# Optimization experiments

Hardware: AMD Instinct MI355X
Metric: run time of the kernel (lower is better)

Reference implementation:

```python
import jax, jax.numpy as jnp
import numpy as np

B, C, RES, N_ANGLES = 32, 16, 128, 64


def setup_inputs() -> dict:
    key = jax.random.key(0)
    k1, k2, k3 = jax.random.split(key, 3)
    x = jax.random.normal(k1, (B, C, RES, RES), dtype=jnp.float32)
    # torch-radon setup: angles = np.linspace(0, 2*pi, 64)
    angles = jnp.linspace(0.0, 2.0 * np.pi, N_ANGLES).astype(jnp.float32)
    # Conv2d(16, 1, 1) params (kaiming-ish scale)
    conv_w = jax.random.normal(k2, (1, C, 1, 1), dtype=jnp.float32) * (1.0 / np.sqrt(C))
    conv_b = jax.random.normal(k3, (1,), dtype=jnp.float32) * 0.01
    return {"x": x, "angles": angles, "conv_w": conv_w, "conv_b": conv_b}


def _radon(x, angles):
    # x: (B, C, H, W) -> sinogram (B, C, n_angles, det_count)
    H = x.shape[-2]
    W = x.shape[-1]
    center = (H - 1) / 2.0
    # detector positions s and ray-integration positions t, in pixel units, centered
    coords = jnp.arange(H, dtype=jnp.float32) - center  # (RES,)

    def proj_one(carry, theta):
        c, s = jnp.cos(theta), jnp.sin(theta)
        # rotated sampling grid: (D, T) = (detector, along-ray)
        xs = coords[:, None] * c - coords[None, :] * s + center
        ys = coords[:, None] * s + coords[None, :] * c + center
        x0 = jnp.floor(xs)
        y0 = jnp.floor(ys)
        wx = xs - x0  # bilinear weights
        wy = ys - y0
        x0i = x0.astype(jnp.int32)
        y0i = y0.astype(jnp.int32)

        def g(yi, xi):
            # zero-padded gather: (B, C, D, T)
            valid = ((yi >= 0) & (yi < H) & (xi >= 0) & (xi < W)).astype(x.dtype)
            v = x[:, :, jnp.clip(yi, 0, H - 1), jnp.clip(xi, 0, W - 1)]
            return v * valid

        val = (g(y0i, x0i) * ((1.0 - wy) * (1.0 - wx))
               + g(y0i, x0i + 1) * ((1.0 - wy) * wx)
               + g(y0i + 1, x0i) * (wy * (1.0 - wx))
               + g(y0i + 1, x0i + 1) * (wy * wx))
        # line integral: sum along the ray (T axis) -> (B, C, D)
        return carry, val.sum(axis=-1)

    _, sino = jax.lax.scan(proj_one, 0, angles)  # (A, B, C, D)
    return jnp.transpose(sino, (1, 2, 0, 3))      # (B, C, A, D)


def reference(x, angles, conv_w, conv_b):
    sino = _radon(x, angles)  # (B, C, A, D)
    # 1x1 conv: contract channel dim
    out = jnp.einsum('bcad,oc->boad', sino, conv_w[:, :, 0, 0])
    return out + conv_b[None, :, None, None]
```

## Files before the change

### kernel.cpp

```cpp
#include <hip/hip_runtime.h>


#define B_   32
#define C_   16
#define RES  128
#define NA   64
#define SLDS 133
#define ROWS 132
#define LDSZ (ROWS * SLDS)

__global__ __launch_bounds__(256) void chan_reduce(const float* __restrict__ x,
                                                   const float* __restrict__ w,
                                                   float* __restrict__ y) {
    int t  = blockIdx.x * 256 + threadIdx.x;
    int b  = t >> 12;
    int r4 = t & 4095;
    const float4* xb = (const float4*)(x + (size_t)b * C_ * RES * RES);
    float wr[C_];
#pragma unroll
    for (int c = 0; c < C_; ++c) wr[c] = w[c];
    float4 acc = make_float4(0.f, 0.f, 0.f, 0.f);
#pragma unroll
    for (int c = 0; c < C_; ++c) {
        float4 v = xb[c * (RES * RES / 4) + r4];
        acc.x = fmaf(wr[c], v.x, acc.x);
        acc.y = fmaf(wr[c], v.y, acc.y);
        acc.z = fmaf(wr[c], v.z, acc.z);
        acc.w = fmaf(wr[c], v.w, acc.w);
    }
    ((float4*)y)[(size_t)b * (RES * RES / 4) + r4] = acc;
}

__global__ __launch_bounds__(512) void radon_k(const float* __restrict__ y,
                                               const float* __restrict__ angles,
                                               const float* __restrict__ bias,
                                               float* __restrict__ out) {
    __shared__ float lds[LDSZ];
    const int bid = blockIdx.x;
    const int b   = bid >> 4;
    const int grp = bid & 15;
    const int t   = threadIdx.x;

    {
        float2* l2 = (float2*)lds;
#pragma unroll
        for (int p = 0; p < 18; ++p) {
            int idx = p * 512 + t;
            if (idx < LDSZ / 2) l2[idx] = make_float2(0.f, 0.f);
        }
        if (t == 0) lds[LDSZ - 1] = 0.f;
    }
    __syncthreads();

    {
        const float* yb = y + (size_t)b * RES * RES;
#pragma unroll
        for (int p = 0; p < 8; ++p) {
            int q = p * 512 + t;
            int r = q >> 5;
            int c = (q & 31) << 2;
            float4 v = *(const float4*)(yb + r * RES + c);
            float* d = &lds[(r + 2) * SLDS + (c + 2)];
            d[0] = v.x; d[1] = v.y; d[2] = v.z; d[3] = v.w;
        }
    }
    __syncthreads();

    const int a = grp * 4 + (t >> 7);
    const int i = t & 127;
    float th = angles[a];
    float s, c;
    __sincosf(th, &s, &c);

    const float ci = (float)i - 63.5f;
    const float Xi = fmaf(ci, c, 65.5f);
    const float Yi = fmaf(ci, s, 65.5f);

    float acc = 0.0f;
#pragma unroll 8
    for (int j = 0; j < RES; ++j) {
        float cj = (float)j - 63.5f;
        float X  = fmaf(cj, -s, Xi);
        float Y  = fmaf(cj,  c, Yi);
        float fx = floorf(X), fy = floorf(Y);
        float wx = X - fx,    wy = Y - fy;
        float gx = fminf(fmaxf(fx, 0.0f), 130.0f);
        float gy = fminf(fmaxf(fy, 0.0f), 130.0f);
        int addr = (int)fmaf(gy, (float)SLDS, gx);
        const float* p0 = &lds[addr];
        float v00 = p0[0],    v01 = p0[1];
        float v10 = p0[SLDS], v11 = p0[SLDS + 1];
        float h0 = fmaf(wx, v01 - v00, v00);
        float h1 = fmaf(wx, v11 - v10, v10);
        acc = acc + fmaf(wy, h1 - h0, h0);
    }

    out[b * (NA * RES) + a * RES + i] = acc + bias[0];
}

extern "C" void kernel_launch(void* const* d_in, const int* in_sizes, int n_in,
                              void* d_out, int out_size, void* d_ws, size_t ws_size,
                              hipStream_t stream) {
    const float* x      = (const float*)d_in[0];
    const float* angles = (const float*)d_in[1];
    const float* w      = (const float*)d_in[2];
    const float* bias   = (const float*)d_in[3];
    float* out = (float*)d_out;
    float* y   = (float*)d_ws;

    chan_reduce<<<dim3(512), dim3(256), 0, stream>>>(x, w, y);
    radon_k<<<dim3(B_ * 16), dim3(512), 0, stream>>>(y, angles, bias, out);
}
```

Before: 106.6 us.

## Store image in LDS as fp16 neighbor pairs and use packed dot2 bilinear

The shared-memory image is now stored as half2 pairs holding each pixel together with its right neighbor. The bilinear tap then needs two LDS loads instead of four, and interpolation becomes two v_dot2 instructions with packed fp16 weights. Two accumulators and a larger unroll are added to shorten the dependency chain. This is meant to cut LDS traffic and ALU work in the inner ray loop. In exchange, image values and weights are rounded to fp16, which adds error.

```diff
diff --git a/kernel.cpp b/kernel.cpp
--- a/kernel.cpp
+++ b/kernel.cpp
@@ -8,6 +8,8 @@
 #define SLDS 133
 #define ROWS 132
 #define LDSZ (ROWS * SLDS)
+
+typedef _Float16 half2v __attribute__((ext_vector_type(2)));
 
 __global__ __launch_bounds__(256) void chan_reduce(const float* __restrict__ x,
                                                    const float* __restrict__ w,
@@ -35,7 +37,7 @@
                                                const float* __restrict__ angles,
                                                const float* __restrict__ bias,
                                                float* __restrict__ out) {
-    __shared__ float lds[LDSZ];
+    __shared__ half2v lds[LDSZ];
     const int bid = blockIdx.x;
     const int b   = bid >> 4;
     const int grp = bid & 15;
@@ -48,7 +50,6 @@
             int idx = p * 512 + t;
             if (idx < LDSZ / 2) l2[idx] = make_float2(0.f, 0.f);
         }
-        if (t == 0) lds[LDSZ - 1] = 0.f;
     }
     __syncthreads();
 
@@ -58,10 +59,16 @@
         for (int p = 0; p < 8; ++p) {
             int q = p * 512 + t;
             int r = q >> 5;
-            int c = (q & 31) << 2;
-            float4 v = *(const float4*)(yb + r * RES + c);
-            float* d = &lds[(r + 2) * SLDS + (c + 2)];
-            d[0] = v.x; d[1] = v.y; d[2] = v.z; d[3] = v.w;
+            int k = q & 31;
+            float4 v = *(const float4*)(yb + r * RES + (k << 2));
+            float v4 = (k < 31) ? yb[r * RES + (k << 2) + 4] : 0.f;
+            half2v* row = &lds[(r + 2) * SLDS];
+            int c0 = (k << 2) + 2;
+            row[c0]     = half2v{(_Float16)v.x, (_Float16)v.y};
+            row[c0 + 1] = half2v{(_Float16)v.y, (_Float16)v.z};
+            row[c0 + 2] = half2v{(_Float16)v.z, (_Float16)v.w};
+            row[c0 + 3] = half2v{(_Float16)v.w, (_Float16)v4};
+            if (k == 0) row[1] = half2v{(_Float16)0.f, (_Float16)v.x};
         }
     }
     __syncthreads();
@@ -76,8 +83,8 @@
     const float Xi = fmaf(ci, c, 65.5f);
     const float Yi = fmaf(ci, s, 65.5f);
 
-    float acc = 0.0f;
-#pragma unroll 8
+    float acc0 = 0.0f, acc1 = 0.0f;
+#pragma unroll 16
     for (int j = 0; j < RES; ++j) {
         float cj = (float)j - 63.5f;
         float X  = fmaf(cj, -s, Xi);
@@ -87,15 +94,17 @@
         float gx = fminf(fmaxf(fx, 0.0f), 130.0f);
         float gy = fminf(fmaxf(fy, 0.0f), 130.0f);
         int addr = (int)fmaf(gy, (float)SLDS, gx);
-        const float* p0 = &lds[addr];
-        float v00 = p0[0],    v01 = p0[1];
-        float v10 = p0[SLDS], v11 = p0[SLDS + 1];
-        float h0 = fmaf(wx, v01 - v00, v00);
-        float h1 = fmaf(wx, v11 - v10, v10);
-        acc = acc + fmaf(wy, h1 - h0, h0);
+        half2v p0 = lds[addr];
+        half2v p1 = lds[addr + SLDS];
+        float u  = 1.0f - wx;
+        float A0 = 1.0f - wy;
+        half2v wa = __builtin_bit_cast(half2v, __builtin_amdgcn_cvt_pkrtz(A0 * u, A0 * wx));
+        half2v wb = __builtin_bit_cast(half2v, __builtin_amdgcn_cvt_pkrtz(wy * u, wy * wx));
+        acc0 = __builtin_amdgcn_fdot2(p0, wa, acc0, false);
+        acc1 = __builtin_amdgcn_fdot2(p1, wb, acc1, false);
     }
 
-    out[b * (NA * RES) + a * RES + i] = acc + bias[0];
+    out[b * (NA * RES) + a * RES + i] = (acc0 + acc1) + bias[0];
 }
 
 extern "C" void kernel_launch(void* const* d_in, const int* in_sizes, int n_in,
```

Measured after the change: 101.8 us. -4.4%, faster.

## Pack batch pairs into fp16 horizontal pairs and use fdot2 bilinear sampling

Applied to the files above, without the earlier changes.

Adds a pack kernel that stores each padded pixel as fp16 horizontal neighbour pairs for two batch images at once. The radon kernel then samples two images per thread, using two LDS uint2 loads and packed fp16 dot products instead of four fp32 loads and lerps per image. This halves the grid, cuts LDS reads per sample, and replaces the in-kernel zeroing and padding with a plain copy. In exchange it adds a third kernel launch and a global workspace round trip, and fp16 rounding of both pixel values and weights lowers accuracy.

```diff
diff --git a/kernel.cpp b/kernel.cpp
--- a/kernel.cpp
+++ b/kernel.cpp
@@ -1,13 +1,17 @@
 #include <hip/hip_runtime.h>
 
 
-#define B_   32
-#define C_   16
-#define RES  128
-#define NA   64
-#define SLDS 133
-#define ROWS 132
-#define LDSZ (ROWS * SLDS)
+#define B_    32
+#define C_    16
+#define RES   128
+#define NA    64
+#define SLDS  133
+#define ROWS  132
+#define NELEM (ROWS * SLDS)
+#define NPAD  18432
+#define NPAIR 16
+
+typedef _Float16 half2v __attribute__((ext_vector_type(2)));
 
 __global__ __launch_bounds__(256) void chan_reduce(const float* __restrict__ x,
                                                    const float* __restrict__ w,
@@ -31,71 +35,86 @@
     ((float4*)y)[(size_t)b * (RES * RES / 4) + r4] = acc;
 }
 
-__global__ __launch_bounds__(512) void radon_k(const float* __restrict__ y,
+__global__ __launch_bounds__(256) void pack_pairs(const float* __restrict__ y,
+                                                  uint2* __restrict__ pk) {
+    int flat = blockIdx.x * 256 + threadIdx.x;
+    int p    = flat / NPAD;
+    int rem  = flat - p * NPAD;
+    uint2 val = make_uint2(0u, 0u);
+    if (rem < NELEM) {
+        int r = rem / SLDS;
+        int c = rem - r * SLDS;
+        if (r >= 2 && r <= 129 && c >= 1 && c <= 129) {
+            int q = r - 2;
+            int m = c - 2;
+            const float* y0 = y + (size_t)(2 * p) * (RES * RES) + q * RES;
+            const float* y1 = y0 + RES * RES;
+            float a0 = (m >= 0)  ? y0[m]     : 0.f;
+            float a1 = (m < 127) ? y0[m + 1] : 0.f;
+            float b0 = (m >= 0)  ? y1[m]     : 0.f;
+            float b1 = (m < 127) ? y1[m + 1] : 0.f;
+            val.x = __builtin_bit_cast(unsigned int, __builtin_amdgcn_cvt_pkrtz(a0, a1));
+            val.y = __builtin_bit_cast(unsigned int, __builtin_amdgcn_cvt_pkrtz(b0, b1));
+        }
+    }
+    pk[flat] = val;
+}
+
+__global__ __launch_bounds__(512) void radon_k(const uint2* __restrict__ pk,
                                                const float* __restrict__ angles,
                                                const float* __restrict__ bias,
                                                float* __restrict__ out) {
-    __shared__ float lds[LDSZ];
+    __shared__ uint2 lds[NPAD];
     const int bid = blockIdx.x;
-    const int b   = bid >> 4;
+    const int p   = bid >> 4;
     const int grp = bid & 15;
     const int t   = threadIdx.x;
 
     {
-        float2* l2 = (float2*)lds;
+        const uint4* src = (const uint4*)(pk + (size_t)p * NPAD);
+        uint4*       dst = (uint4*)lds;
 #pragma unroll
-        for (int p = 0; p < 18; ++p) {
-            int idx = p * 512 + t;
-            if (idx < LDSZ / 2) l2[idx] = make_float2(0.f, 0.f);
-        }
-        if (t == 0) lds[LDSZ - 1] = 0.f;
+        for (int k = 0; k < 18; ++k) dst[k * 512 + t] = src[k * 512 + t];
     }
     __syncthreads();
 
-    {
-        const float* yb = y + (size_t)b * RES * RES;
-#pragma unroll
-        for (int p = 0; p < 8; ++p) {
-            int q = p * 512 + t;
-            int r = q >> 5;
-            int c = (q & 31) << 2;
-            float4 v = *(const float4*)(yb + r * RES + c);
-            float* d = &lds[(r + 2) * SLDS + (c + 2)];
-            d[0] = v.x; d[1] = v.y; d[2] = v.z; d[3] = v.w;
-        }
-    }
-    __syncthreads();
-
-    const int a = grp * 4 + (t >> 7);
+    const int a = (t >> 7) * 16 + grp;
     const int i = t & 127;
     float th = angles[a];
     float s, c;
     __sincosf(th, &s, &c);
 
     const float ci = (float)i - 63.5f;
-    const float Xi = fmaf(ci, c, 65.5f);
-    const float Yi = fmaf(ci, s, 65.5f);
+    const float Xb = fmaf(ci, c, fmaf(63.5f, s, 65.5f));
+    const float Yb = fmaf(ci, s, fmaf(-63.5f, c, 65.5f));
+    const float ns = -s;
 
-    float acc = 0.0f;
+    float acc00 = 0.f, acc01 = 0.f, acc10 = 0.f, acc11 = 0.f;
 #pragma unroll 8
     for (int j = 0; j < RES; ++j) {
-        float cj = (float)j - 63.5f;
-        float X  = fmaf(cj, -s, Xi);
-        float Y  = fmaf(cj,  c, Yi);
+        float jf = (float)j;
+        float X  = fmaf(jf, ns, Xb);
+        float Y  = fmaf(jf, c,  Yb);
         float fx = floorf(X), fy = floorf(Y);
         float wx = X - fx,    wy = Y - fy;
-        float gx = fminf(fmaxf(fx, 0.0f), 130.0f);
-        float gy = fminf(fmaxf(fy, 0.0f), 130.0f);
+        float gx = fminf(fmaxf(fx, 0.f), 130.f);
+        float gy = fminf(fmaxf(fy, 0.f), 130.f);
         int addr = (int)fmaf(gy, (float)SLDS, gx);
-        const float* p0 = &lds[addr];
-        float v00 = p0[0],    v01 = p0[1];
-        float v10 = p0[SLDS], v11 = p0[SLDS + 1];
-        float h0 = fmaf(wx, v01 - v00, v00);
-        float h1 = fmaf(wx, v11 - v10, v10);
-        acc = acc + fmaf(wy, h1 - h0, h0);
+        uint2 q0 = lds[addr];
+        uint2 q1 = lds[addr + SLDS];
+        float u  = 1.f - wx;
+        float A0 = 1.f - wy;
+        half2v wa = __builtin_bit_cast(half2v, __builtin_amdgcn_cvt_pkrtz(A0 * u, A0 * wx));
+        half2v wb = __builtin_bit_cast(half2v, __builtin_amdgcn_cvt_pkrtz(wy * u, wy * wx));
+        acc00 = __builtin_amdgcn_fdot2(__builtin_bit_cast(half2v, q0.x), wa, acc00, false);
+        acc10 = __builtin_amdgcn_fdot2(__builtin_bit_cast(half2v, q0.y), wa, acc10, false);
+        acc01 = __builtin_amdgcn_fdot2(__builtin_bit_cast(half2v, q1.x), wb, acc01, false);
+        acc11 = __builtin_amdgcn_fdot2(__builtin_bit_cast(half2v, q1.y), wb, acc11, false);
     }
 
-    out[b * (NA * RES) + a * RES + i] = acc + bias[0];
+    float bv = bias[0];
+    out[(2 * p)     * (NA * RES) + a * RES + i] = (acc00 + acc01) + bv;
+    out[(2 * p + 1) * (NA * RES) + a * RES + i] = (acc10 + acc11) + bv;
 }
 
 extern "C" void kernel_launch(void* const* d_in, const int* in_sizes, int n_in,
@@ -106,8 +125,11 @@
     const float* w      = (const float*)d_in[2];
     const float* bias   = (const float*)d_in[3];
     float* out = (float*)d_out;
-    float* y   = (float*)d_ws;
+
+    float* y  = (float*)d_ws;
+    uint2* pk = (uint2*)((char*)d_ws + (size_t)4 * 1024 * 1024);
 
     chan_reduce<<<dim3(512), dim3(256), 0, stream>>>(x, w, y);
-    radon_k<<<dim3(B_ * 16), dim3(512), 0, stream>>>(y, angles, bias, out);
+    pack_pairs<<<dim3(NPAIR * NPAD / 256), dim3(256), 0, stream>>>(y, pk);
+    radon_k<<<dim3(NPAIR * 16), dim3(512), 0, stream>>>(pk, angles, bias, out);
 }
```

Result: faster. 98.05 us (-8.0%).
